# Optimization experiments

Measured on AMD Instinct MI355X. Metric: run time of the kernel, lower is better.

The kernel has to match this reference:

```python
import jax, jax.numpy as jnp
import numpy as np

M, N, DIM = 256, 256, 512
NITER = 1000
ALPHA = 0.3
SIGMA = max(M, N) / 2.0  # matches torch default sigma = max(m, n) / 2


def _locations():
    # Row-major 2-D grid coordinates, same order as SOM.neuron_locations()
    ii, jj = jnp.meshgrid(jnp.arange(M), jnp.arange(N), indexing='ij')
    return jnp.stack([ii.ravel(), jj.ravel()], axis=1)  # (M*N, 2) int32


def setup_inputs() -> dict:
    key = jax.random.key(0)
    k1, k2 = jax.random.split(key)
    return {
        'x': jax.random.normal(k1, (DIM,), dtype=jnp.float32),
        'weights': jax.random.normal(k2, (M * N, DIM), dtype=jnp.float32),
        'y': 3,     # label, only used for stats in the original; not in the math
        'it': 100,  # current iteration, controls alpha/sigma decay
    }


def reference(x, weights, y, it):
    locs = _locations()                                   # (M*N, 2)
    # BMU search: L2 distance from x to every neuron, argmin
    dists = jnp.linalg.norm(weights - x[None, :], axis=1)  # (M*N,)
    bmu_index = jnp.argmin(dists)
    bmu_loc = locs[bmu_index]                             # (2,)
    # Faithful to original: bmu_loc[0]*m + bmu_loc[1] (m == n here)
    bmu_1d = bmu_loc[0] * M + bmu_loc[1]
    winner = weights[bmu_1d]                              # (DIM,)
    # Linearly decaying learning rate / neighbourhood radius
    lr = 1.0 - it / NITER
    alpha_op = ALPHA * lr
    sigma_op = SIGMA * lr
    # Gaussian neighbourhood over squared grid distance to BMU
    d2 = jnp.sum((locs.astype(jnp.float32) - bmu_loc.astype(jnp.float32)) ** 2, axis=1)  # (M*N,)
    neigh = jnp.exp(-d2 / (sigma_op ** 2))
    # Weight update: w += alpha * h(i, bmu) * (x - w)
    new_weights = weights + (alpha_op * neigh)[:, None] * (x[None, :] - weights)
    return winner, new_weights
```

## Files before the change

### kernel.cpp

```cpp
#include <hip/hip_runtime.h>
#include <stdint.h>

#define DIMD 512
#define ROWS 65536

#define K_BLOCKS 2048
#define WPB      4
#define RPW      8

typedef float vfloat4 __attribute__((ext_vector_type(4)));

__global__ __launch_bounds__(256) void som_argmin_kernel(
    const float* __restrict__ x,
    const float* __restrict__ w,
    unsigned long long* __restrict__ slots)
{
    const int lane  = threadIdx.x & 63;
    const int wave  = threadIdx.x >> 6;
    const int gwave = blockIdx.x * WPB + wave;
    const int row0  = gwave * RPW;

    const float4* x4 = reinterpret_cast<const float4*>(x);
    const float4 xa = x4[lane];
    const float4 xb = x4[lane + 64];

    float d[RPW];

    #pragma unroll
    for (int r = 0; r < RPW; ++r) {
        const float4* w4 =
            reinterpret_cast<const float4*>(w + (size_t)(row0 + r) * DIMD);
        const float4 wa = w4[lane];
        const float4 wb = w4[lane + 64];

        float s = 0.0f, t;
        t = wa.x - xa.x; s = fmaf(t, t, s);
        t = wa.y - xa.y; s = fmaf(t, t, s);
        t = wa.z - xa.z; s = fmaf(t, t, s);
        t = wa.w - xa.w; s = fmaf(t, t, s);
        t = wb.x - xb.x; s = fmaf(t, t, s);
        t = wb.y - xb.y; s = fmaf(t, t, s);
        t = wb.z - xb.z; s = fmaf(t, t, s);
        t = wb.w - xb.w; s = fmaf(t, t, s);
        d[r] = s;
    }

    #pragma unroll
    for (int off = 32; off > 0; off >>= 1) {
        #pragma unroll
        for (int r = 0; r < RPW; ++r)
            d[r] += __shfl_xor(d[r], off, 64);
    }

    unsigned long long best = ~0ull;
    #pragma unroll
    for (int r = 0; r < RPW; ++r) {
        unsigned long long key =
            (((unsigned long long)__float_as_uint(d[r])) << 32) |
            (unsigned long long)(unsigned)(row0 + r);
        best = (key < best) ? key : best;
    }

    __shared__ unsigned long long sbest[WPB];
    if (lane == 0) sbest[wave] = best;
    __syncthreads();
    if (threadIdx.x == 0) {
        unsigned long long b = sbest[0];
        #pragma unroll
        for (int i = 1; i < WPB; ++i) b = (sbest[i] < b) ? sbest[i] : b;
        slots[blockIdx.x] = b;
    }
}

__global__ __launch_bounds__(256) void som_update_kernel(
    const float* __restrict__ x,
    const float* __restrict__ w,
    const int* __restrict__ it_ptr,
    const unsigned long long* __restrict__ slots,
    float* __restrict__ out)
{
    const int lane = threadIdx.x & 63;
    const int wave = threadIdx.x >> 6;

    unsigned long long b = ~0ull;
    for (int i = threadIdx.x; i < K_BLOCKS; i += 256) {
        unsigned long long v = slots[i];
        b = (v < b) ? v : b;
    }
    #pragma unroll
    for (int off = 32; off > 0; off >>= 1) {
        unsigned long long o = __shfl_xor(b, off, 64);
        b = (o < b) ? o : b;
    }
    __shared__ unsigned long long sbest[WPB];
    if (lane == 0) sbest[wave] = b;
    __syncthreads();
    unsigned long long g = sbest[0];
    #pragma unroll
    for (int i = 1; i < WPB; ++i) g = (sbest[i] < g) ? sbest[i] : g;

    const unsigned bmu = (unsigned)(g & 0xFFFFFFFFull);
    const float bi = (float)(bmu >> 8);
    const float bj = (float)(bmu & 255u);

    const double itd      = (double)(*it_ptr);
    const double lr       = 1.0 - itd / 1000.0;
    const float  alpha_op = (float)(0.3 * lr);
    const double sigma_op = 128.0 * lr;
    const float  inv_s2   = (float)(1.0 / (sigma_op * sigma_op));

    const float4* x4 = reinterpret_cast<const float4*>(x);
    const float4 xa = x4[lane];
    const float4 xb = x4[lane + 64];

    float* winner      = out;
    float* new_weights = out + DIMD;

    const int rblk  = (K_BLOCKS - 1) - blockIdx.x;
    const int gwave = rblk * WPB + wave;
    const int row0  = gwave * RPW;

    #pragma unroll
    for (int r = 0; r < RPW; ++r) {
        const int row = row0 + r;
        const float di = (float)(row >> 8) - bi;
        const float dj = (float)(row & 255) - bj;
        const float coef = alpha_op * __expf(-(di * di + dj * dj) * inv_s2);

        const float4* w4 =
            reinterpret_cast<const float4*>(w + (size_t)row * DIMD);
        const float4 wa = w4[lane];
        const float4 wb = w4[lane + 64];

        vfloat4 oa, ob;
        oa.x = fmaf(coef, xa.x - wa.x, wa.x);
        oa.y = fmaf(coef, xa.y - wa.y, wa.y);
        oa.z = fmaf(coef, xa.z - wa.z, wa.z);
        oa.w = fmaf(coef, xa.w - wa.w, wa.w);
        ob.x = fmaf(coef, xb.x - wb.x, wb.x);
        ob.y = fmaf(coef, xb.y - wb.y, wb.y);
        ob.z = fmaf(coef, xb.z - wb.z, wb.z);
        ob.w = fmaf(coef, xb.w - wb.w, wb.w);

        vfloat4* o4 = reinterpret_cast<vfloat4*>(new_weights + (size_t)row * DIMD);
        __builtin_nontemporal_store(oa, o4 + lane);
        __builtin_nontemporal_store(ob, o4 + lane + 64);

        if (row == (int)bmu) {
            float4* wn = reinterpret_cast<float4*>(winner);
            wn[lane]      = wa;
            wn[lane + 64] = wb;
        }
    }
}

extern "C" void kernel_launch(void* const* d_in, const int* in_sizes, int n_in,
                              void* d_out, int out_size, void* d_ws, size_t ws_size,
                              hipStream_t stream) {
    const float* x       = (const float*)d_in[0];
    const float* weights = (const float*)d_in[1];
    const int*   it_ptr  = (const int*)d_in[3];

    float* out = (float*)d_out;
    unsigned long long* slots = (unsigned long long*)d_ws;

    som_argmin_kernel<<<K_BLOCKS, 256, 0, stream>>>(x, weights, slots);
    som_update_kernel<<<K_BLOCKS, 256, 0, stream>>>(x, weights, it_ptr, slots, out);
}
```

Baseline: 69.99 us.

## Fuse argmin and update into one persistent kernel with grid barrier and LDS row cache

Merges the BMU search and the weight update into a single kernel of 1024 blocks, each wave handling 16 rows, with an atomic-counter grid barrier between the two phases. The first three rows per wave are kept in LDS so they are not re-read from memory during the update, and the remaining rows are re-read from global memory, where they may still hit in L2 or MALL. The aim is to drop the second launch and some of the re-read traffic. In exchange it adds a memset, a spin barrier that relies on all 1024 blocks being co-resident, and 24KB of LDS per block, which may reduce occupancy.

```diff
diff --git a/kernel.cpp b/kernel.cpp
--- a/kernel.cpp
+++ b/kernel.cpp
@@ -4,100 +4,164 @@
 #define DIMD 512
 #define ROWS 65536
 
-#define K_BLOCKS 2048
-#define WPB      4
-#define RPW      8
+#define GRID  1024
+#define BLOCK 256
+#define WPB   4
+#define RPW   16
+#define LDSR  3
 
 typedef float vfloat4 __attribute__((ext_vector_type(4)));
 
-__global__ __launch_bounds__(256) void som_argmin_kernel(
+__device__ __forceinline__ float dist8(const float4 wa, const float4 wb,
+                                       const float4 xa, const float4 xb)
+{
+    float s = 0.0f, t;
+    t = wa.x - xa.x; s = fmaf(t, t, s);
+    t = wa.y - xa.y; s = fmaf(t, t, s);
+    t = wa.z - xa.z; s = fmaf(t, t, s);
+    t = wa.w - xa.w; s = fmaf(t, t, s);
+    t = wb.x - xb.x; s = fmaf(t, t, s);
+    t = wb.y - xb.y; s = fmaf(t, t, s);
+    t = wb.z - xb.z; s = fmaf(t, t, s);
+    t = wb.w - xb.w; s = fmaf(t, t, s);
+    return s;
+}
+
+__device__ __forceinline__ void update_row(const float4 wa, const float4 wb,
+                                           const float4 xa, const float4 xb,
+                                           int row, unsigned bmu,
+                                           float bi, float bj,
+                                           float alpha_op, float inv_s2,
+                                           float* __restrict__ winner,
+                                           float* __restrict__ new_weights,
+                                           int lane)
+{
+    const float di = (float)(row >> 8) - bi;
+    const float dj = (float)(row & 255) - bj;
+    const float coef = alpha_op * __expf(-(di * di + dj * dj) * inv_s2);
+
+    vfloat4 oa, ob;
+    oa.x = fmaf(coef, xa.x - wa.x, wa.x);
+    oa.y = fmaf(coef, xa.y - wa.y, wa.y);
+    oa.z = fmaf(coef, xa.z - wa.z, wa.z);
+    oa.w = fmaf(coef, xa.w - wa.w, wa.w);
+    ob.x = fmaf(coef, xb.x - wb.x, wb.x);
+    ob.y = fmaf(coef, xb.y - wb.y, wb.y);
+    ob.z = fmaf(coef, xb.z - wb.z, wb.z);
+    ob.w = fmaf(coef, xb.w - wb.w, wb.w);
+
+    vfloat4* o4 = reinterpret_cast<vfloat4*>(new_weights + (size_t)row * DIMD);
+    __builtin_nontemporal_store(oa, o4 + lane);
+    __builtin_nontemporal_store(ob, o4 + lane + 64);
+
+    if (row == (int)bmu) {
+        float4* wn = reinterpret_cast<float4*>(winner);
+        wn[lane]      = wa;
+        wn[lane + 64] = wb;
+    }
+}
+
+__global__ __launch_bounds__(BLOCK, 8) void som_fused(
     const float* __restrict__ x,
     const float* __restrict__ w,
-    unsigned long long* __restrict__ slots)
+    const int* __restrict__ it_ptr,
+    unsigned long long* __restrict__ slots,
+    int* __restrict__ done,
+    float* __restrict__ out)
 {
-    const int lane  = threadIdx.x & 63;
-    const int wave  = threadIdx.x >> 6;
-    const int gwave = blockIdx.x * WPB + wave;
-    const int row0  = gwave * RPW;
+    __shared__ float lds[WPB * LDSR * DIMD];
+    __shared__ unsigned long long sred[WPB];
+
+    const int lane = threadIdx.x & 63;
+    const int wave = threadIdx.x >> 6;
+    const int row0 = (blockIdx.x * WPB + wave) * RPW;
 
     const float4* x4 = reinterpret_cast<const float4*>(x);
     const float4 xa = x4[lane];
     const float4 xb = x4[lane + 64];
-
-    float d[RPW];
-
-    #pragma unroll
-    for (int r = 0; r < RPW; ++r) {
-        const float4* w4 =
-            reinterpret_cast<const float4*>(w + (size_t)(row0 + r) * DIMD);
-        const float4 wa = w4[lane];
-        const float4 wb = w4[lane + 64];
-
-        float s = 0.0f, t;
-        t = wa.x - xa.x; s = fmaf(t, t, s);
-        t = wa.y - xa.y; s = fmaf(t, t, s);
-        t = wa.z - xa.z; s = fmaf(t, t, s);
-        t = wa.w - xa.w; s = fmaf(t, t, s);
-        t = wb.x - xb.x; s = fmaf(t, t, s);
-        t = wb.y - xb.y; s = fmaf(t, t, s);
-        t = wb.z - xb.z; s = fmaf(t, t, s);
-        t = wb.w - xb.w; s = fmaf(t, t, s);
-        d[r] = s;
-    }
-
+    const float4* w4 = reinterpret_cast<const float4*>(w);
+
+    unsigned long long best = ~0ull;
+    float d[8];
+
+    #pragma unroll
+    for (int r = 0; r < 8; ++r) {
+        const float4* p = w4 + (size_t)(row0 + r) * (DIMD / 4);
+        const float4 wa  = p[lane];
+        const float4 wbv = p[lane + 64];
+        if (r < LDSR) {
+            float4* dst = reinterpret_cast<float4*>(
+                lds + (wave * LDSR + r) * DIMD);
+            dst[lane]      = wa;
+            dst[lane + 64] = wbv;
+        }
+        d[r] = dist8(wa, wbv, xa, xb);
+    }
     #pragma unroll
     for (int off = 32; off > 0; off >>= 1) {
         #pragma unroll
-        for (int r = 0; r < RPW; ++r)
-            d[r] += __shfl_xor(d[r], off, 64);
-    }
-
-    unsigned long long best = ~0ull;
-    #pragma unroll
-    for (int r = 0; r < RPW; ++r) {
-        unsigned long long key =
+        for (int r = 0; r < 8; ++r) d[r] += __shfl_xor(d[r], off, 64);
+    }
+    #pragma unroll
+    for (int r = 0; r < 8; ++r) {
+        const unsigned long long key =
             (((unsigned long long)__float_as_uint(d[r])) << 32) |
             (unsigned long long)(unsigned)(row0 + r);
         best = (key < best) ? key : best;
     }
 
-    __shared__ unsigned long long sbest[WPB];
-    if (lane == 0) sbest[wave] = best;
+    #pragma unroll
+    for (int r = 0; r < 8; ++r) {
+        const float4* p = w4 + (size_t)(row0 + 8 + r) * (DIMD / 4);
+        d[r] = dist8(p[lane], p[lane + 64], xa, xb);
+    }
+    #pragma unroll
+    for (int off = 32; off > 0; off >>= 1) {
+        #pragma unroll
+        for (int r = 0; r < 8; ++r) d[r] += __shfl_xor(d[r], off, 64);
+    }
+    #pragma unroll
+    for (int r = 0; r < 8; ++r) {
+        const unsigned long long key =
+            (((unsigned long long)__float_as_uint(d[r])) << 32) |
+            (unsigned long long)(unsigned)(row0 + 8 + r);
+        best = (key < best) ? key : best;
+    }
+
+    if (lane == 0) sred[wave] = best;
     __syncthreads();
     if (threadIdx.x == 0) {
-        unsigned long long b = sbest[0];
+        unsigned long long b = sred[0];
         #pragma unroll
-        for (int i = 1; i < WPB; ++i) b = (sbest[i] < b) ? sbest[i] : b;
-        slots[blockIdx.x] = b;
-    }
-}
-
-__global__ __launch_bounds__(256) void som_update_kernel(
-    const float* __restrict__ x,
-    const float* __restrict__ w,
-    const int* __restrict__ it_ptr,
-    const unsigned long long* __restrict__ slots,
-    float* __restrict__ out)
-{
-    const int lane = threadIdx.x & 63;
-    const int wave = threadIdx.x >> 6;
-
-    unsigned long long b = ~0ull;
-    for (int i = threadIdx.x; i < K_BLOCKS; i += 256) {
-        unsigned long long v = slots[i];
-        b = (v < b) ? v : b;
+        for (int i = 1; i < WPB; ++i) b = (sred[i] < b) ? sred[i] : b;
+        __hip_atomic_store(&slots[blockIdx.x], b, __ATOMIC_RELEASE,
+                           __HIP_MEMORY_SCOPE_AGENT);
+        __hip_atomic_fetch_add(done, 1, __ATOMIC_ACQ_REL,
+                               __HIP_MEMORY_SCOPE_AGENT);
+        while (__hip_atomic_load(done, __ATOMIC_ACQUIRE,
+                                 __HIP_MEMORY_SCOPE_AGENT) < GRID) {
+            __builtin_amdgcn_s_sleep(2);
+        }
+        __threadfence();
+    }
+    __syncthreads();
+
+    unsigned long long g = ~0ull;
+    #pragma unroll
+    for (int k = 0; k < GRID / BLOCK; ++k) {
+        const unsigned long long v = slots[k * BLOCK + threadIdx.x];
+        g = (v < g) ? v : g;
     }
     #pragma unroll
     for (int off = 32; off > 0; off >>= 1) {
-        unsigned long long o = __shfl_xor(b, off, 64);
-        b = (o < b) ? o : b;
-    }
-    __shared__ unsigned long long sbest[WPB];
-    if (lane == 0) sbest[wave] = b;
+        const unsigned long long o = __shfl_xor(g, off, 64);
+        g = (o < g) ? o : g;
+    }
+    if (lane == 0) sred[wave] = g;
     __syncthreads();
-    unsigned long long g = sbest[0];
-    #pragma unroll
-    for (int i = 1; i < WPB; ++i) g = (sbest[i] < g) ? sbest[i] : g;
+    g = sred[0];
+    #pragma unroll
+    for (int i = 1; i < WPB; ++i) g = (sred[i] < g) ? sred[i] : g;
 
     const unsigned bmu = (unsigned)(g & 0xFFFFFFFFull);
     const float bi = (float)(bmu >> 8);
@@ -109,48 +173,22 @@
     const double sigma_op = 128.0 * lr;
     const float  inv_s2   = (float)(1.0 / (sigma_op * sigma_op));
 
-    const float4* x4 = reinterpret_cast<const float4*>(x);
-    const float4 xa = x4[lane];
-    const float4 xb = x4[lane + 64];
-
     float* winner      = out;
     float* new_weights = out + DIMD;
 
-    const int rblk  = (K_BLOCKS - 1) - blockIdx.x;
-    const int gwave = rblk * WPB + wave;
-    const int row0  = gwave * RPW;
-
-    #pragma unroll
-    for (int r = 0; r < RPW; ++r) {
-        const int row = row0 + r;
-        const float di = (float)(row >> 8) - bi;
-        const float dj = (float)(row & 255) - bj;
-        const float coef = alpha_op * __expf(-(di * di + dj * dj) * inv_s2);
-
-        const float4* w4 =
-            reinterpret_cast<const float4*>(w + (size_t)row * DIMD);
-        const float4 wa = w4[lane];
-        const float4 wb = w4[lane + 64];
-
-        vfloat4 oa, ob;
-        oa.x = fmaf(coef, xa.x - wa.x, wa.x);
-        oa.y = fmaf(coef, xa.y - wa.y, wa.y);
-        oa.z = fmaf(coef, xa.z - wa.z, wa.z);
-        oa.w = fmaf(coef, xa.w - wa.w, wa.w);
-        ob.x = fmaf(coef, xb.x - wb.x, wb.x);
-        ob.y = fmaf(coef, xb.y - wb.y, wb.y);
-        ob.z = fmaf(coef, xb.z - wb.z, wb.z);
-        ob.w = fmaf(coef, xb.w - wb.w, wb.w);
-
-        vfloat4* o4 = reinterpret_cast<vfloat4*>(new_weights + (size_t)row * DIMD);
-        __builtin_nontemporal_store(oa, o4 + lane);
-        __builtin_nontemporal_store(ob, o4 + lane + 64);
-
-        if (row == (int)bmu) {
-            float4* wn = reinterpret_cast<float4*>(winner);
-            wn[lane]      = wa;
-            wn[lane + 64] = wb;
-        }
+    #pragma unroll 2
+    for (int r = LDSR; r < RPW; ++r) {
+        const float4* p = w4 + (size_t)(row0 + r) * (DIMD / 4);
+        update_row(p[lane], p[lane + 64], xa, xb, row0 + r, bmu,
+                   bi, bj, alpha_op, inv_s2, winner, new_weights, lane);
+    }
+
+    #pragma unroll
+    for (int r = 0; r < LDSR; ++r) {
+        const float4* src = reinterpret_cast<const float4*>(
+            lds + (wave * LDSR + r) * DIMD);
+        update_row(src[lane], src[lane + 64], xa, xb, row0 + r, bmu,
+                   bi, bj, alpha_op, inv_s2, winner, new_weights, lane);
     }
 }
 
@@ -162,8 +200,11 @@
     const int*   it_ptr  = (const int*)d_in[3];
 
     float* out = (float*)d_out;
-    unsigned long long* slots = (unsigned long long*)d_ws;
-
-    som_argmin_kernel<<<K_BLOCKS, 256, 0, stream>>>(x, weights, slots);
-    som_update_kernel<<<K_BLOCKS, 256, 0, stream>>>(x, weights, it_ptr, slots, out);
-}
+
+    int*                done  = (int*)d_ws;
+    unsigned long long* slots = (unsigned long long*)((char*)d_ws + 64);
+
+    hipMemsetAsync(done, 0, sizeof(int), stream);
+
+    som_fused<<<GRID, BLOCK, 0, stream>>>(x, weights, it_ptr, slots, done, out);
+}
```

Measured after the change: 221.2 us. 3.16x slower.
